# Kernel tuning notes

Measured on AMD Instinct MI355X. Metric: run time of the kernel, lower is better.

Reference implementation:

```python
import jax, jax.numpy as jnp
import numpy as np

V, T, E, H, L, R = 50257, 1024, 768, 12, 6, 4
B = 2
D = E // H
NEG = -1e9


def layer_norm(x, w, b, eps=1e-5):
    m = jnp.mean(x, axis=-1, keepdims=True)
    v = jnp.var(x, axis=-1, keepdims=True)
    return (x - m) * jax.lax.rsqrt(v + eps) * w + b


def setup_inputs() -> dict:
    key = jax.random.key(0)
    ks = jax.random.split(key, 8)
    s = 0.02
    inp = {
        "x": jax.random.randint(ks[0], (B, T), 0, V, dtype=jnp.int64),
        "tok_emb": s * jax.random.normal(ks[1], (V, E), jnp.float32),
        "pos_emb": s * jax.random.normal(ks[2], (T, E), jnp.float32),
        "ln1_w": jnp.ones((L, E), jnp.float32),
        "ln1_b": jnp.zeros((L, E), jnp.float32),
        "qkv_w": s * jax.random.normal(ks[3], (L, E, 3 * E), jnp.float32),
        "qkv_b": jnp.zeros((L, 3 * E), jnp.float32),
        "out_w": s * jax.random.normal(ks[4], (L, E, E), jnp.float32),
        "out_b": jnp.zeros((L, E), jnp.float32),
        "ln2_w": jnp.ones((L, E), jnp.float32),
        "ln2_b": jnp.zeros((L, E), jnp.float32),
        "mlp_w1": s * jax.random.normal(ks[5], (L, E, R * E), jnp.float32),
        "mlp_b1": jnp.zeros((L, R * E), jnp.float32),
        "mlp_w2": s * jax.random.normal(ks[6], (L, R * E, E), jnp.float32),
        "mlp_b2": jnp.zeros((L, E), jnp.float32),
        "lnf_w": jnp.ones((E,), jnp.float32),
        "lnf_b": jnp.zeros((E,), jnp.float32),
        "head_w": s * jax.random.normal(ks[7], (E, V), jnp.float32),
    }
    return inp


def _gpt2(x, tok_emb, pos_emb, ln1_w, ln1_b, qkv_w, qkv_b, out_w, out_b,
          ln2_w, ln2_b, mlp_w1, mlp_b1, mlp_w2, mlp_b2, lnf_w, lnf_b, head_w):
    b, t = x.shape
    h = tok_emb[x] + pos_emb[:t][None]  # [B,T,E]; dropout = identity (eval)
    mask = jnp.tril(jnp.ones((t, t), bool))
    scale = 1.0 / np.sqrt(D)

    def block(h, p):
        l1w, l1b, qw, qb, ow, ob, l2w, l2b, w1, b1, w2, b2 = p
        hn = layer_norm(h, l1w, l1b)
        qkv = hn @ qw + qb  # [B,T,3E]
        q, k, v = jnp.split(qkv, 3, axis=-1)
        q = q.reshape(b, t, H, D).transpose(0, 2, 1, 3)  # [B,H,T,D]
        k = k.reshape(b, t, H, D).transpose(0, 2, 1, 3)
        v = v.reshape(b, t, H, D).transpose(0, 2, 1, 3)
        att = jnp.einsum('bhqd,bhkd->bhqk', q, k) * scale
        att = jnp.where(mask, att, NEG)
        att = jax.nn.softmax(att, axis=-1)  # att dropout = identity (eval)
        o = jnp.einsum('bhqk,bhkd->bhqd', att, v)
        o = o.transpose(0, 2, 1, 3).reshape(b, t, E)
        h = h + (o @ ow + ob)  # res dropout = identity
        hn2 = layer_norm(h, l2w, l2b)
        m = jax.nn.gelu(hn2 @ w1 + b1, approximate=False) @ w2 + b2
        return h + m, None

    layer_params = (ln1_w, ln1_b, qkv_w, qkv_b, out_w, out_b,
                    ln2_w, ln2_b, mlp_w1, mlp_b1, mlp_w2, mlp_b2)
    h, _ = jax.lax.scan(block, h, layer_params)
    h = layer_norm(h, lnf_w, lnf_b)
    return h @ head_w  # [B,T,V]


def reference(x, tok_emb, pos_emb, ln1_w, ln1_b, qkv_w, qkv_b, out_w, out_b,
              ln2_w, ln2_b, mlp_w1, mlp_b1, mlp_w2, mlp_b2, lnf_w, lnf_b, head_w):
    return _gpt2(x, tok_emb, pos_emb, ln1_w, ln1_b, qkv_w, qkv_b, out_w, out_b,
                 ln2_w, ln2_b, mlp_w1, mlp_b1, mlp_w2, mlp_b2, lnf_w, lnf_b, head_w)
```

## Files before the change

kernel.cpp:

```cpp
#include <hip/hip_runtime.h>
#include <hip/hip_bf16.h>
#include <math.h>
#include <stdint.h>


#define T_SEQ 1024
#define E_DIM 768
#define NHEAD 12
#define HDIM 64
#define NLAYER 6
#define VOCAB 50257
#define VPAD 50304
#define BT 2048

typedef __attribute__((ext_vector_type(8))) short bf16x8;
typedef __attribute__((ext_vector_type(4))) float f32x4;

static __device__ __forceinline__ ushort f2bf(float x) {
    uint u = __float_as_uint(x);
    uint r = (u + 0x7fffu + ((u >> 16) & 1u)) >> 16;
    return (ushort)r;
}
static __device__ __forceinline__ float bf2f(ushort u) {
    return __uint_as_float(((uint)u) << 16);
}

static __device__ __forceinline__ void gld16(const ushort* g, ushort* l) {
    __builtin_amdgcn_global_load_lds(
        (const __attribute__((address_space(1))) void*)g,
        (__attribute__((address_space(3))) void*)l, 16, 0, 0);
}

__global__ __launch_bounds__(192) void embed_k(const int* __restrict__ x,
                                               const float* __restrict__ tok,
                                               const float* __restrict__ pos,
                                               float* __restrict__ h) {
    int bt = blockIdx.x;
    int t = bt & (T_SEQ - 1);
    int id = x[bt];
    float4 a = ((const float4*)(tok + (size_t)id * E_DIM))[threadIdx.x];
    float4 b = ((const float4*)(pos + (size_t)t * E_DIM))[threadIdx.x];
    float4 r; r.x = a.x + b.x; r.y = a.y + b.y; r.z = a.z + b.z; r.w = a.w + b.w;
    ((float4*)(h + (size_t)bt * E_DIM))[threadIdx.x] = r;
}

__global__ __launch_bounds__(256) void ln_k(const float* __restrict__ in,
                                            const float* __restrict__ w,
                                            const float* __restrict__ b,
                                            ushort* __restrict__ oh,
                                            ushort* __restrict__ ol) {
    int rid = blockIdx.x;
    int tid = threadIdx.x;
    const float* rp = in + (size_t)rid * E_DIM;
    float x0 = rp[tid], x1 = rp[tid + 256], x2 = rp[tid + 512];
    float s = x0 + x1 + x2;
    float q = x0 * x0 + x1 * x1 + x2 * x2;
    #pragma unroll
    for (int off = 32; off >= 1; off >>= 1) {
        s += __shfl_down(s, off);
        q += __shfl_down(q, off);
    }
    __shared__ float ss[4], qq[4];
    int lane = tid & 63, wid = tid >> 6;
    if (lane == 0) { ss[wid] = s; qq[wid] = q; }
    __syncthreads();
    float S = ss[0] + ss[1] + ss[2] + ss[3];
    float Q = qq[0] + qq[1] + qq[2] + qq[3];
    float mean = S * (1.0f / E_DIM);
    float var = Q * (1.0f / E_DIM) - mean * mean;
    float inv = rsqrtf(var + 1e-5f);
    size_t ob = (size_t)rid * E_DIM;
    #pragma unroll
    for (int j = 0; j < 3; j++) {
        int c = tid + j * 256;
        float xv = (j == 0) ? x0 : (j == 1) ? x1 : x2;
        float y = (xv - mean) * inv * w[c] + b[c];
        ushort hh = f2bf(y);
        oh[ob + c] = hh;
        ol[ob + c] = f2bf(y - bf2f(hh));
    }
}

__global__ __launch_bounds__(256) void tconv_k(const float* __restrict__ W,
                                               ushort* __restrict__ Thi,
                                               ushort* __restrict__ Tlo,
                                               int K, int N, int Npad) {
    int k0 = blockIdx.x * 32, n0 = blockIdx.y * 32;
    __shared__ float tile[32][33];
    int t = threadIdx.x;
    int kr = t >> 3, nc = (t & 7) << 2;
    const float* wp = W + (size_t)(k0 + kr) * N + n0 + nc;
    #pragma unroll
    for (int j = 0; j < 4; j++)
        tile[kr][nc + j] = (n0 + nc + j < N) ? wp[j] : 0.f;
    __syncthreads();
    int nr = t >> 3, kc = (t & 7) << 2;
    ushort hv[4], lv[4];
    #pragma unroll
    for (int j = 0; j < 4; j++) {
        float x = tile[kc + j][nr];
        hv[j] = f2bf(x);
        lv[j] = f2bf(x - bf2f(hv[j]));
    }
    size_t ob = (size_t)(n0 + nr) * K + k0 + kc;
    uint2 ph, pl;
    ph.x = (uint)hv[0] | ((uint)hv[1] << 16); ph.y = (uint)hv[2] | ((uint)hv[3] << 16);
    pl.x = (uint)lv[0] | ((uint)lv[1] << 16); pl.y = (uint)lv[2] | ((uint)lv[3] << 16);
    *(uint2*)(Thi + ob) = ph;
    *(uint2*)(Tlo + ob) = pl;
}

template <int EPI>
__global__ __launch_bounds__(256) void gemmf_k(const ushort* __restrict__ Ahi,
                                               const ushort* __restrict__ Alo,
                                               const ushort* __restrict__ Bhi,
                                               const ushort* __restrict__ Blo,
                                               const float* __restrict__ bias,
                                               const float* __restrict__ res,
                                               float* __restrict__ C,
                                               ushort* __restrict__ Chi,
                                               ushort* __restrict__ Clo,
                                               int M, int N, int K) {
    __shared__ __align__(16) ushort lds[4 * 128 * 32];
    ushort* Ash = lds;
    ushort* Asl = lds + 4096;
    ushort* Bsh = lds + 8192;
    ushort* Bsl = lds + 12288;
    const int tid = threadIdx.x;
    const int lane = tid & 63;
    const int wave = tid >> 6;
    const int wm64 = (wave >> 1) * 64;
    const int wn64 = (wave & 1) * 64;
    const int lrow = lane & 15;
    const int lkc = lane >> 4;
    const int n0 = blockIdx.x * 128;
    const int m0 = blockIdx.y * 128;

    f32x4 acc[4][4];
    #pragma unroll
    for (int i = 0; i < 4; i++)
        #pragma unroll
        for (int j = 0; j < 4; j++)
            acc[i][j] = (f32x4){0.f, 0.f, 0.f, 0.f};

    const int r0s = wave * 16 + (lane >> 2);
    const int r1s = r0s + 64;
    const int c0s = ((lane & 3) ^ ((r0s >> 1) & 3)) << 3;
    const int c1s = ((lane & 3) ^ ((r1s >> 1) & 3)) << 3;
    const ushort* pAh0 = Ahi + (size_t)(m0 + r0s) * K + c0s;
    const ushort* pAh1 = Ahi + (size_t)(m0 + r1s) * K + c1s;
    const ushort* pAl0 = Alo + (size_t)(m0 + r0s) * K + c0s;
    const ushort* pAl1 = Alo + (size_t)(m0 + r1s) * K + c1s;
    const ushort* pBh0 = Bhi + (size_t)(n0 + r0s) * K + c0s;
    const ushort* pBh1 = Bhi + (size_t)(n0 + r1s) * K + c1s;
    const ushort* pBl0 = Blo + (size_t)(n0 + r0s) * K + c0s;
    const ushort* pBl1 = Blo + (size_t)(n0 + r1s) * K + c1s;
    ushort* dst0 = lds + (size_t)wave * 512;
    ushort* dst1 = lds + (size_t)(wave + 4) * 512;

    for (int k0 = 0; k0 < K; k0 += 32) {
        __syncthreads();
        gld16(pAh0 + k0, dst0);
        gld16(pAh1 + k0, dst1);
        gld16(pAl0 + k0, dst0 + 4096);
        gld16(pAl1 + k0, dst1 + 4096);
        gld16(pBh0 + k0, dst0 + 8192);
        gld16(pBh1 + k0, dst1 + 8192);
        gld16(pBl0 + k0, dst0 + 12288);
        gld16(pBl1 + k0, dst1 + 12288);
        __syncthreads();

        bf16x8 ah[4], al[4], bh[4], bl[4];
        #pragma unroll
        for (int f = 0; f < 4; f++) {
            int arow = wm64 + (f << 4) + lrow;
            int aoff = (arow << 5) + ((lkc ^ ((arow >> 1) & 3)) << 3);
            ah[f] = *(const bf16x8*)&Ash[aoff];
            al[f] = *(const bf16x8*)&Asl[aoff];
            int brow = wn64 + (f << 4) + lrow;
            int boff = (brow << 5) + ((lkc ^ ((brow >> 1) & 3)) << 3);
            bh[f] = *(const bf16x8*)&Bsh[boff];
            bl[f] = *(const bf16x8*)&Bsl[boff];
        }
        #pragma unroll
        for (int mf = 0; mf < 4; mf++)
            #pragma unroll
            for (int nf = 0; nf < 4; nf++) {
                acc[mf][nf] = __builtin_amdgcn_mfma_f32_16x16x32_bf16(
                    ah[mf], bh[nf], acc[mf][nf], 0, 0, 0);
                acc[mf][nf] = __builtin_amdgcn_mfma_f32_16x16x32_bf16(
                    ah[mf], bl[nf], acc[mf][nf], 0, 0, 0);
                acc[mf][nf] = __builtin_amdgcn_mfma_f32_16x16x32_bf16(
                    al[mf], bh[nf], acc[mf][nf], 0, 0, 0);
            }
    }

    const int colb = n0 + wn64 + (lane & 15);
    const int rowb = m0 + wm64 + ((lane >> 4) << 2);
    #pragma unroll
    for (int nf = 0; nf < 4; nf++) {
        int col = colb + nf * 16;
        if (col >= N) continue;
        float bv = bias ? bias[col] : 0.f;
        #pragma unroll
        for (int mf = 0; mf < 4; mf++) {
            f32x4 v = acc[mf][nf];
            #pragma unroll
            for (int q = 0; q < 4; q++) {
                int row = rowb + mf * 16 + q;
                size_t idx = (size_t)row * N + col;
                float x = v[q] + bv;
                if (EPI == 1) {
                    x = 0.5f * x * (1.0f + erff(x * 0.70710678118654752f));
                    ushort hh = f2bf(x);
                    Chi[idx] = hh;
                    Clo[idx] = f2bf(x - bf2f(hh));
                } else if (EPI == 2) {
                    x += res[idx];
                    C[idx] = x;
                } else {
                    C[idx] = x;
                }
            }
        }
    }
}

__global__ __launch_bounds__(256) void attn_k(const float* __restrict__ qkv,
                                              ushort* __restrict__ oh,
                                              ushort* __restrict__ ol) {
    const int qt = blockIdx.x;
    const int hh = blockIdx.y;
    const int bb = blockIdx.z;
    const int tid = threadIdx.x;
    __shared__ __align__(16) float Qs[64][68];
    __shared__ __align__(16) float Ks[64][68];
    __shared__ __align__(16) float Vs[64][68];
    __shared__ __align__(16) float Ssm[64][68];
    __shared__ float m_s[64], l_s[64], f_s[64];

    const int q0 = qt * 64;
    const size_t base = (size_t)bb * T_SEQ * (3 * E_DIM);
    const int hoff = hh * HDIM;

    #pragma unroll
    for (int j = 0; j < 4; j++) {
        int s = tid + j * 256;
        int rr = s >> 4, c4 = (s & 15) << 2;
        *(float4*)&Qs[rr][c4] =
            *(const float4*)(qkv + base + (size_t)(q0 + rr) * (3 * E_DIM) + hoff + c4);
    }
    if (tid < 64) { m_s[tid] = -1e30f; l_s[tid] = 0.f; }

    float acc[4][4] = {};
    const int r0 = (tid >> 4) << 2, c0 = (tid & 15) << 2;
    const int rs = tid >> 2, cq = (tid & 3) << 4;

    for (int kt = 0; kt <= qt; ++kt) {
        int k0 = kt * 64;
        __syncthreads();
        #pragma unroll
        for (int j = 0; j < 4; j++) {
            int s = tid + j * 256;
            int rr = s >> 4, c4 = (s & 15) << 2;
            const float* kp = qkv + base + (size_t)(k0 + rr) * (3 * E_DIM) + hoff;
            *(float4*)&Ks[rr][c4] = *(const float4*)(kp + E_DIM + c4);
            *(float4*)&Vs[rr][c4] = *(const float4*)(kp + 2 * E_DIM + c4);
        }
        __syncthreads();

        float sacc[4][4] = {};
        #pragma unroll
        for (int d0 = 0; d0 < 64; d0 += 4) {
            float qf[4][4], kf[4][4];
            #pragma unroll
            for (int i = 0; i < 4; i++) {
                float4 v = *(const float4*)&Qs[r0 + i][d0];
                qf[i][0] = v.x; qf[i][1] = v.y; qf[i][2] = v.z; qf[i][3] = v.w;
            }
            #pragma unroll
            for (int j = 0; j < 4; j++) {
                float4 v = *(const float4*)&Ks[c0 + j][d0];
                kf[j][0] = v.x; kf[j][1] = v.y; kf[j][2] = v.z; kf[j][3] = v.w;
            }
            #pragma unroll
            for (int i = 0; i < 4; i++)
                #pragma unroll
                for (int j = 0; j < 4; j++)
                    #pragma unroll
                    for (int d = 0; d < 4; d++)
                        sacc[i][j] = fmaf(qf[i][d], kf[j][d], sacc[i][j]);
        }
        bool diag = (kt == qt);
        #pragma unroll
        for (int i = 0; i < 4; i++) {
            float4 w;
            float vv[4];
            #pragma unroll
            for (int j = 0; j < 4; j++) {
                float v = sacc[i][j] * 0.125f;
                if (diag && (c0 + j) > (r0 + i)) v = -1e9f;
                vv[j] = v;
            }
            w.x = vv[0]; w.y = vv[1]; w.z = vv[2]; w.w = vv[3];
            *(float4*)&Ssm[r0 + i][c0] = w;
        }
        __syncthreads();

        float mx = -1e30f;
        #pragma unroll
        for (int c = 0; c < 16; c++) mx = fmaxf(mx, Ssm[rs][cq + c]);
        mx = fmaxf(mx, __shfl_xor(mx, 1));
        mx = fmaxf(mx, __shfl_xor(mx, 2));
        float m_old = m_s[rs];
        float m_new = fmaxf(m_old, mx);
        float ps = 0.f;
        #pragma unroll
        for (int c = 0; c < 16; c++) {
            float p = expf(Ssm[rs][cq + c] - m_new);
            Ssm[rs][cq + c] = p;
            ps += p;
        }
        ps += __shfl_xor(ps, 1);
        ps += __shfl_xor(ps, 2);
        if ((tid & 3) == 0) {
            float f = expf(m_old - m_new);
            l_s[rs] = l_s[rs] * f + ps;
            m_s[rs] = m_new;
            f_s[rs] = f;
        }
        __syncthreads();

        #pragma unroll
        for (int i = 0; i < 4; i++) {
            float f = f_s[r0 + i];
            #pragma unroll
            for (int j = 0; j < 4; j++) acc[i][j] *= f;
        }
        #pragma unroll 8
        for (int k = 0; k < 64; k++) {
            float4 vv = *(const float4*)&Vs[k][c0];
            float vf[4] = {vv.x, vv.y, vv.z, vv.w};
            float pv[4];
            #pragma unroll
            for (int i = 0; i < 4; i++) pv[i] = Ssm[r0 + i][k];
            #pragma unroll
            for (int i = 0; i < 4; i++)
                #pragma unroll
                for (int j = 0; j < 4; j++)
                    acc[i][j] = fmaf(pv[i], vf[j], acc[i][j]);
        }
    }

    #pragma unroll
    for (int i = 0; i < 4; i++) {
        float inv = 1.0f / l_s[r0 + i];
        size_t idx = (size_t)(bb * T_SEQ + q0 + r0 + i) * E_DIM + hoff + c0;
        ushort hv[4], lv[4];
        #pragma unroll
        for (int j = 0; j < 4; j++) {
            float v = acc[i][j] * inv;
            hv[j] = f2bf(v);
            lv[j] = f2bf(v - bf2f(hv[j]));
        }
        uint2 ph, pl;
        ph.x = (uint)hv[0] | ((uint)hv[1] << 16); ph.y = (uint)hv[2] | ((uint)hv[3] << 16);
        pl.x = (uint)lv[0] | ((uint)lv[1] << 16); pl.y = (uint)lv[2] | ((uint)lv[3] << 16);
        *(uint2*)(oh + idx) = ph;
        *(uint2*)(ol + idx) = pl;
    }
}

static inline char* al256(char* p) {
    return (char*)(((uintptr_t)p + 255) & ~(uintptr_t)255);
}

extern "C" void kernel_launch(void* const* d_in, const int* in_sizes, int n_in,
                              void* d_out, int out_size, void* d_ws, size_t ws_size,
                              hipStream_t stream) {
    const int* x        = (const int*)d_in[0];
    const float* tok    = (const float*)d_in[1];
    const float* pos    = (const float*)d_in[2];
    const float* ln1_w  = (const float*)d_in[3];
    const float* ln1_b  = (const float*)d_in[4];
    const float* qkv_w  = (const float*)d_in[5];
    const float* qkv_b  = (const float*)d_in[6];
    const float* out_w  = (const float*)d_in[7];
    const float* out_b  = (const float*)d_in[8];
    const float* ln2_w  = (const float*)d_in[9];
    const float* ln2_b  = (const float*)d_in[10];
    const float* mlp_w1 = (const float*)d_in[11];
    const float* mlp_b1 = (const float*)d_in[12];
    const float* mlp_w2 = (const float*)d_in[13];
    const float* mlp_b2 = (const float*)d_in[14];
    const float* lnf_w  = (const float*)d_in[15];
    const float* lnf_b  = (const float*)d_in[16];
    const float* head_w = (const float*)d_in[17];
    float* out = (float*)d_out;

    char* p = (char*)d_ws;
    float* h    = (float*)p;  p = al256(p + (size_t)BT * E_DIM * 4);
    float* qkvb = (float*)p;  p = al256(p + (size_t)BT * 3 * E_DIM * 4);
    ushort* hnh = (ushort*)p; p = al256(p + (size_t)BT * E_DIM * 2);
    ushort* hnl = (ushort*)p; p = al256(p + (size_t)BT * E_DIM * 2);
    ushort* obh = (ushort*)p; p = al256(p + (size_t)BT * E_DIM * 2);
    ushort* obl = (ushort*)p; p = al256(p + (size_t)BT * E_DIM * 2);
    ushort* m1h = (ushort*)p; p = al256(p + (size_t)BT * 4 * E_DIM * 2);
    ushort* m1l = (ushort*)p; p = al256(p + (size_t)BT * 4 * E_DIM * 2);
    ushort* qTh = (ushort*)p; p = al256(p + (size_t)3 * E_DIM * E_DIM * 2);
    ushort* qTl = (ushort*)p; p = al256(p + (size_t)3 * E_DIM * E_DIM * 2);
    ushort* oTh = (ushort*)p; p = al256(p + (size_t)E_DIM * E_DIM * 2);
    ushort* oTl = (ushort*)p; p = al256(p + (size_t)E_DIM * E_DIM * 2);
    ushort* w1h = (ushort*)p; p = al256(p + (size_t)4 * E_DIM * E_DIM * 2);
    ushort* w1l = (ushort*)p; p = al256(p + (size_t)4 * E_DIM * E_DIM * 2);
    ushort* w2h = (ushort*)p; p = al256(p + (size_t)4 * E_DIM * E_DIM * 2);
    ushort* w2l = (ushort*)p; p = al256(p + (size_t)4 * E_DIM * E_DIM * 2);
    ushort* hTh = (ushort*)p; p = al256(p + (size_t)VPAD * E_DIM * 2);
    ushort* hTl = (ushort*)p; p = al256(p + (size_t)VPAD * E_DIM * 2);

    embed_k<<<BT, 192, 0, stream>>>(x, tok, pos, h);

    for (int l = 0; l < NLAYER; ++l) {
        tconv_k<<<dim3(E_DIM / 32, 3 * E_DIM / 32), 256, 0, stream>>>(
            qkv_w + (size_t)l * E_DIM * 3 * E_DIM, qTh, qTl,
            E_DIM, 3 * E_DIM, 3 * E_DIM);
        tconv_k<<<dim3(E_DIM / 32, E_DIM / 32), 256, 0, stream>>>(
            out_w + (size_t)l * E_DIM * E_DIM, oTh, oTl, E_DIM, E_DIM, E_DIM);
        tconv_k<<<dim3(E_DIM / 32, 4 * E_DIM / 32), 256, 0, stream>>>(
            mlp_w1 + (size_t)l * E_DIM * 4 * E_DIM, w1h, w1l,
            E_DIM, 4 * E_DIM, 4 * E_DIM);
        tconv_k<<<dim3(4 * E_DIM / 32, E_DIM / 32), 256, 0, stream>>>(
            mlp_w2 + (size_t)l * 4 * E_DIM * E_DIM, w2h, w2l,
            4 * E_DIM, E_DIM, E_DIM);

        ln_k<<<BT, 256, 0, stream>>>(h, ln1_w + l * E_DIM, ln1_b + l * E_DIM,
                                     hnh, hnl);
        gemmf_k<0><<<dim3(3 * E_DIM / 128, BT / 128), 256, 0, stream>>>(
            hnh, hnl, qTh, qTl, qkv_b + (size_t)l * 3 * E_DIM, nullptr,
            qkvb, nullptr, nullptr, BT, 3 * E_DIM, E_DIM);
        attn_k<<<dim3(T_SEQ / 64, NHEAD, 2), 256, 0, stream>>>(qkvb, obh, obl);
        gemmf_k<2><<<dim3(E_DIM / 128, BT / 128), 256, 0, stream>>>(
            obh, obl, oTh, oTl, out_b + (size_t)l * E_DIM, h,
            h, nullptr, nullptr, BT, E_DIM, E_DIM);
        ln_k<<<BT, 256, 0, stream>>>(h, ln2_w + l * E_DIM, ln2_b + l * E_DIM,
                                     hnh, hnl);
        gemmf_k<1><<<dim3(4 * E_DIM / 128, BT / 128), 256, 0, stream>>>(
            hnh, hnl, w1h, w1l, mlp_b1 + (size_t)l * 4 * E_DIM, nullptr,
            nullptr, m1h, m1l, BT, 4 * E_DIM, E_DIM);
        gemmf_k<2><<<dim3(E_DIM / 128, BT / 128), 256, 0, stream>>>(
            m1h, m1l, w2h, w2l, mlp_b2 + (size_t)l * E_DIM, h,
            h, nullptr, nullptr, BT, E_DIM, 4 * E_DIM);
    }

    tconv_k<<<dim3(E_DIM / 32, VPAD / 32), 256, 0, stream>>>(
        head_w, hTh, hTl, E_DIM, VOCAB, VPAD);
    ln_k<<<BT, 256, 0, stream>>>(h, lnf_w, lnf_b, hnh, hnl);
    gemmf_k<0><<<dim3(VPAD / 128, BT / 128), 256, 0, stream>>>(
        hnh, hnl, hTh, hTl, nullptr, nullptr,
        out, nullptr, nullptr, BT, VOCAB, E_DIM);
}
```

Baseline: 4.478 ms.

## Split-K small GEMMs, batch weight conversion, swizzle GEMM blocks, vectorize attention softmax

The output-projection and MLP-down GEMMs now use split-K (2 and 8 slices) writing partial sums, which a new reduction kernel adds to the residual together with the bias. These GEMMs previously launched only 96 workgroups. When the workspace is large enough, all layers' weight transposes and conversions run in batched launches up front instead of per layer. GEMM workgroups are remapped across groups of 8 for better cache locality, and the attention softmax and PV loops use float4 LDS accesses with __expf. The cost is extra partial-sum traffic, an added reduction kernel, and slightly less precise exponentials.

```diff
diff --git a/kernel.cpp b/kernel.cpp
--- a/kernel.cpp
+++ b/kernel.cpp
@@ -85,6 +85,10 @@
                                                ushort* __restrict__ Thi,
                                                ushort* __restrict__ Tlo,
                                                int K, int N, int Npad) {
+    int l = blockIdx.z;
+    W   += (size_t)l * K * N;
+    Thi += (size_t)l * Npad * K;
+    Tlo += (size_t)l * Npad * K;
     int k0 = blockIdx.x * 32, n0 = blockIdx.y * 32;
     __shared__ float tile[32][33];
     int t = threadIdx.x;
@@ -133,8 +137,19 @@
     const int wn64 = (wave & 1) * 64;
     const int lrow = lane & 15;
     const int lkc = lane >> 4;
-    const int n0 = blockIdx.x * 128;
-    const int m0 = blockIdx.y * 128;
+
+    int gx = gridDim.x, gy = gridDim.y;
+    int nwg = gx * gy;
+    int lin = blockIdx.y * gx + blockIdx.x;
+    int bx, by;
+    if ((nwg & 7) == 0) {
+        int chunk = nwg >> 3;
+        int logical = (lin & 7) * chunk + (lin >> 3);
+        bx = logical / gy;
+        by = logical % gy;
+    } else { bx = blockIdx.x; by = blockIdx.y; }
+    const int n0 = bx * 128;
+    const int m0 = by * 128;
 
     f32x4 acc[4][4];
     #pragma unroll
@@ -158,7 +173,15 @@
     ushort* dst0 = lds + (size_t)wave * 512;
     ushort* dst1 = lds + (size_t)(wave + 4) * 512;
 
-    for (int k0 = 0; k0 < K; k0 += 32) {
+    int kz = 0, kbeg = 0, kend = K;
+    if (EPI == 3) {
+        kz = blockIdx.z;
+        int Ks = K / gridDim.z;
+        kbeg = kz * Ks;
+        kend = kbeg + Ks;
+    }
+
+    for (int k0 = kbeg; k0 < kend; k0 += 32) {
         __syncthreads();
         gld16(pAh0 + k0, dst0);
         gld16(pAh1 + k0, dst1);
@@ -197,6 +220,7 @@
 
     const int colb = n0 + wn64 + (lane & 15);
     const int rowb = m0 + wm64 + ((lane >> 4) << 2);
+    const size_t pbase = (EPI == 3) ? (size_t)kz * M * N : 0;
     #pragma unroll
     for (int nf = 0; nf < 4; nf++) {
         int col = colb + nf * 16;
@@ -218,12 +242,30 @@
                 } else if (EPI == 2) {
                     x += res[idx];
                     C[idx] = x;
+                } else if (EPI == 3) {
+                    C[pbase + idx] = x;
                 } else {
                     C[idx] = x;
                 }
             }
         }
     }
+}
+
+__global__ __launch_bounds__(256) void redres_k(const float* __restrict__ P,
+                                                const float* __restrict__ bias,
+                                                float* __restrict__ h,
+                                                int MN, int N, int KZ) {
+    int i = (blockIdx.x * 256 + threadIdx.x) * 4;
+    if (i >= MN) return;
+    float4 s = *(const float4*)(h + i);
+    float4 b = *(const float4*)(bias + (i % N));
+    s.x += b.x; s.y += b.y; s.z += b.z; s.w += b.w;
+    for (int z = 0; z < KZ; z++) {
+        float4 pv = *(const float4*)(P + (size_t)z * MN + i);
+        s.x += pv.x; s.y += pv.y; s.z += pv.z; s.w += pv.w;
+    }
+    *(float4*)(h + i) = s;
 }
 
 __global__ __launch_bounds__(256) void attn_k(const float* __restrict__ qkv,
@@ -307,24 +349,33 @@
         }
         __syncthreads();
 
+        float4 sv[4];
+        #pragma unroll
+        for (int c4 = 0; c4 < 4; c4++)
+            sv[c4] = *(const float4*)&Ssm[rs][cq + c4 * 4];
         float mx = -1e30f;
         #pragma unroll
-        for (int c = 0; c < 16; c++) mx = fmaxf(mx, Ssm[rs][cq + c]);
+        for (int c4 = 0; c4 < 4; c4++)
+            mx = fmaxf(fmaxf(fmaxf(mx, sv[c4].x), fmaxf(sv[c4].y, sv[c4].z)),
+                       sv[c4].w);
         mx = fmaxf(mx, __shfl_xor(mx, 1));
         mx = fmaxf(mx, __shfl_xor(mx, 2));
         float m_old = m_s[rs];
         float m_new = fmaxf(m_old, mx);
         float ps = 0.f;
         #pragma unroll
-        for (int c = 0; c < 16; c++) {
-            float p = expf(Ssm[rs][cq + c] - m_new);
-            Ssm[rs][cq + c] = p;
-            ps += p;
+        for (int c4 = 0; c4 < 4; c4++) {
+            sv[c4].x = __expf(sv[c4].x - m_new);
+            sv[c4].y = __expf(sv[c4].y - m_new);
+            sv[c4].z = __expf(sv[c4].z - m_new);
+            sv[c4].w = __expf(sv[c4].w - m_new);
+            ps += sv[c4].x + sv[c4].y + sv[c4].z + sv[c4].w;
+            *(float4*)&Ssm[rs][cq + c4 * 4] = sv[c4];
         }
         ps += __shfl_xor(ps, 1);
         ps += __shfl_xor(ps, 2);
         if ((tid & 3) == 0) {
-            float f = expf(m_old - m_new);
+            float f = __expf(m_old - m_new);
             l_s[rs] = l_s[rs] * f + ps;
             m_s[rs] = m_new;
             f_s[rs] = f;
@@ -337,18 +388,24 @@
             #pragma unroll
             for (int j = 0; j < 4; j++) acc[i][j] *= f;
         }
-        #pragma unroll 8
-        for (int k = 0; k < 64; k++) {
-            float4 vv = *(const float4*)&Vs[k][c0];
-            float vf[4] = {vv.x, vv.y, vv.z, vv.w};
-            float pv[4];
-            #pragma unroll
-            for (int i = 0; i < 4; i++) pv[i] = Ssm[r0 + i][k];
-            #pragma unroll
-            for (int i = 0; i < 4; i++)
+        #pragma unroll 4
+        for (int k4 = 0; k4 < 64; k4 += 4) {
+            float4 pr[4], vr[4];
+            #pragma unroll
+            for (int i = 0; i < 4; i++) pr[i] = *(const float4*)&Ssm[r0 + i][k4];
+            #pragma unroll
+            for (int d = 0; d < 4; d++) vr[d] = *(const float4*)&Vs[k4 + d][c0];
+            #pragma unroll
+            for (int i = 0; i < 4; i++) {
+                float pf[4] = {pr[i].x, pr[i].y, pr[i].z, pr[i].w};
                 #pragma unroll
-                for (int j = 0; j < 4; j++)
-                    acc[i][j] = fmaf(pv[i], vf[j], acc[i][j]);
+                for (int d = 0; d < 4; d++) {
+                    acc[i][0] = fmaf(pf[d], vr[d].x, acc[i][0]);
+                    acc[i][1] = fmaf(pf[d], vr[d].y, acc[i][1]);
+                    acc[i][2] = fmaf(pf[d], vr[d].z, acc[i][2]);
+                    acc[i][3] = fmaf(pf[d], vr[d].w, acc[i][3]);
+                }
+            }
         }
     }
 
@@ -398,62 +455,145 @@
     const float* head_w = (const float*)d_in[17];
     float* out = (float*)d_out;
 
-    char* p = (char*)d_ws;
-    float* h    = (float*)p;  p = al256(p + (size_t)BT * E_DIM * 4);
-    float* qkvb = (float*)p;  p = al256(p + (size_t)BT * 3 * E_DIM * 4);
-    ushort* hnh = (ushort*)p; p = al256(p + (size_t)BT * E_DIM * 2);
-    ushort* hnl = (ushort*)p; p = al256(p + (size_t)BT * E_DIM * 2);
-    ushort* obh = (ushort*)p; p = al256(p + (size_t)BT * E_DIM * 2);
-    ushort* obl = (ushort*)p; p = al256(p + (size_t)BT * E_DIM * 2);
-    ushort* m1h = (ushort*)p; p = al256(p + (size_t)BT * 4 * E_DIM * 2);
-    ushort* m1l = (ushort*)p; p = al256(p + (size_t)BT * 4 * E_DIM * 2);
-    ushort* qTh = (ushort*)p; p = al256(p + (size_t)3 * E_DIM * E_DIM * 2);
-    ushort* qTl = (ushort*)p; p = al256(p + (size_t)3 * E_DIM * E_DIM * 2);
-    ushort* oTh = (ushort*)p; p = al256(p + (size_t)E_DIM * E_DIM * 2);
-    ushort* oTl = (ushort*)p; p = al256(p + (size_t)E_DIM * E_DIM * 2);
-    ushort* w1h = (ushort*)p; p = al256(p + (size_t)4 * E_DIM * E_DIM * 2);
-    ushort* w1l = (ushort*)p; p = al256(p + (size_t)4 * E_DIM * E_DIM * 2);
-    ushort* w2h = (ushort*)p; p = al256(p + (size_t)4 * E_DIM * E_DIM * 2);
-    ushort* w2l = (ushort*)p; p = al256(p + (size_t)4 * E_DIM * E_DIM * 2);
-    ushort* hTh = (ushort*)p; p = al256(p + (size_t)VPAD * E_DIM * 2);
-    ushort* hTl = (ushort*)p; p = al256(p + (size_t)VPAD * E_DIM * 2);
+    const size_t Zh   = (size_t)BT * E_DIM * 4;
+    const size_t Zqkv = (size_t)BT * 3 * E_DIM * 4;
+    const size_t Zbf  = (size_t)BT * E_DIM * 2;
+    const size_t Zm1  = (size_t)BT * 4 * E_DIM * 2;
+    const size_t ZP   = (size_t)8 * BT * E_DIM * 4;
+    const size_t ZqT  = (size_t)3 * E_DIM * E_DIM * 2;
+    const size_t ZoT  = (size_t)E_DIM * E_DIM * 2;
+    const size_t Zw1T = (size_t)4 * E_DIM * E_DIM * 2;
+    const size_t Zw2T = (size_t)4 * E_DIM * E_DIM * 2;
+    const size_t ZhT  = (size_t)VPAD * E_DIM * 2;
+
+    char* base = (char*)d_ws;
+    char* p = base;
+    auto take = [&](size_t bytes) { char* r = p; p = al256(p + bytes); return r; };
+
+    float*  h    = (float*)take(Zh);
+    float*  qkvb = (float*)take(Zqkv);
+    ushort* hnh  = (ushort*)take(Zbf);
+    ushort* hnl  = (ushort*)take(Zbf);
+    ushort* obh  = (ushort*)take(Zbf);
+    ushort* obl  = (ushort*)take(Zbf);
+    ushort* m1h  = (ushort*)take(Zm1);
+    ushort* m1l  = (ushort*)take(Zm1);
+    float*  Pbuf = (float*)take(ZP);
+    ushort* qTh  = (ushort*)take(ZqT * NLAYER);
+    ushort* qTl  = (ushort*)take(ZqT * NLAYER);
+    ushort* oTh  = (ushort*)take(ZoT * NLAYER);
+    ushort* oTl  = (ushort*)take(ZoT * NLAYER);
+    ushort* w1h  = (ushort*)take(Zw1T * NLAYER);
+    ushort* w1l  = (ushort*)take(Zw1T * NLAYER);
+    ushort* w2h  = (ushort*)take(Zw2T * NLAYER);
+    ushort* w2l  = (ushort*)take(Zw2T * NLAYER);
+    ushort* hTh  = (ushort*)take(ZhT);
+    ushort* hTl  = (ushort*)take(ZhT);
+    bool big = (size_t)(p - base) <= ws_size;
+
+    if (!big) {
+        p = base;
+        h    = (float*)take(Zh);
+        qkvb = (float*)take(Zqkv);
+        hnh  = (ushort*)take(Zbf);
+        hnl  = (ushort*)take(Zbf);
+        obh  = (ushort*)take(Zbf);
+        obl  = (ushort*)take(Zbf);
+        m1h  = (ushort*)take(Zm1);
+        m1l  = (ushort*)take(Zm1);
+        qTh  = (ushort*)take(ZqT);
+        qTl  = (ushort*)take(ZqT);
+        oTh  = (ushort*)take(ZoT);
+        oTl  = (ushort*)take(ZoT);
+        w1h  = (ushort*)take(Zw1T);
+        w1l  = (ushort*)take(Zw1T);
+        w2h  = (ushort*)take(Zw2T);
+        w2l  = (ushort*)take(Zw2T);
+        hTh  = (ushort*)take(ZhT);
+        hTl  = (ushort*)take(ZhT);
+        Pbuf = nullptr;
+    }
+
+    if (big) {
+        tconv_k<<<dim3(E_DIM / 32, 3 * E_DIM / 32, NLAYER), 256, 0, stream>>>(
+            qkv_w, qTh, qTl, E_DIM, 3 * E_DIM, 3 * E_DIM);
+        tconv_k<<<dim3(E_DIM / 32, E_DIM / 32, NLAYER), 256, 0, stream>>>(
+            out_w, oTh, oTl, E_DIM, E_DIM, E_DIM);
+        tconv_k<<<dim3(E_DIM / 32, 4 * E_DIM / 32, NLAYER), 256, 0, stream>>>(
+            mlp_w1, w1h, w1l, E_DIM, 4 * E_DIM, 4 * E_DIM);
+        tconv_k<<<dim3(4 * E_DIM / 32, E_DIM / 32, NLAYER), 256, 0, stream>>>(
+            mlp_w2, w2h, w2l, 4 * E_DIM, E_DIM, E_DIM);
+        tconv_k<<<dim3(E_DIM / 32, VPAD / 32, 1), 256, 0, stream>>>(
+            head_w, hTh, hTl, E_DIM, VOCAB, VPAD);
+    }
 
     embed_k<<<BT, 192, 0, stream>>>(x, tok, pos, h);
 
     for (int l = 0; l < NLAYER; ++l) {
-        tconv_k<<<dim3(E_DIM / 32, 3 * E_DIM / 32), 256, 0, stream>>>(
-            qkv_w + (size_t)l * E_DIM * 3 * E_DIM, qTh, qTl,
-            E_DIM, 3 * E_DIM, 3 * E_DIM);
-        tconv_k<<<dim3(E_DIM / 32, E_DIM / 32), 256, 0, stream>>>(
-            out_w + (size_t)l * E_DIM * E_DIM, oTh, oTl, E_DIM, E_DIM, E_DIM);
-        tconv_k<<<dim3(E_DIM / 32, 4 * E_DIM / 32), 256, 0, stream>>>(
-            mlp_w1 + (size_t)l * E_DIM * 4 * E_DIM, w1h, w1l,
-            E_DIM, 4 * E_DIM, 4 * E_DIM);
-        tconv_k<<<dim3(4 * E_DIM / 32, E_DIM / 32), 256, 0, stream>>>(
-            mlp_w2 + (size_t)l * 4 * E_DIM * E_DIM, w2h, w2l,
-            4 * E_DIM, E_DIM, E_DIM);
+        const ushort *qThl, *qTll, *oThl, *oTll, *w1hl, *w1ll, *w2hl, *w2ll;
+        if (big) {
+            qThl = qTh + (size_t)l * (ZqT / 2);  qTll = qTl + (size_t)l * (ZqT / 2);
+            oThl = oTh + (size_t)l * (ZoT / 2);  oTll = oTl + (size_t)l * (ZoT / 2);
+            w1hl = w1h + (size_t)l * (Zw1T / 2); w1ll = w1l + (size_t)l * (Zw1T / 2);
+            w2hl = w2h + (size_t)l * (Zw2T / 2); w2ll = w2l + (size_t)l * (Zw2T / 2);
+        } else {
+            tconv_k<<<dim3(E_DIM / 32, 3 * E_DIM / 32, 1), 256, 0, stream>>>(
+                qkv_w + (size_t)l * E_DIM * 3 * E_DIM, qTh, qTl,
+                E_DIM, 3 * E_DIM, 3 * E_DIM);
+            tconv_k<<<dim3(E_DIM / 32, E_DIM / 32, 1), 256, 0, stream>>>(
+                out_w + (size_t)l * E_DIM * E_DIM, oTh, oTl, E_DIM, E_DIM, E_DIM);
+            tconv_k<<<dim3(E_DIM / 32, 4 * E_DIM / 32, 1), 256, 0, stream>>>(
+                mlp_w1 + (size_t)l * E_DIM * 4 * E_DIM, w1h, w1l,
+                E_DIM, 4 * E_DIM, 4 * E_DIM);
+            tconv_k<<<dim3(4 * E_DIM / 32, E_DIM / 32, 1), 256, 0, stream>>>(
+                mlp_w2 + (size_t)l * 4 * E_DIM * E_DIM, w2h, w2l,
+                4 * E_DIM, E_DIM, E_DIM);
+            qThl = qTh; qTll = qTl; oThl = oTh; oTll = oTl;
+            w1hl = w1h; w1ll = w1l; w2hl = w2h; w2ll = w2l;
+        }
 
         ln_k<<<BT, 256, 0, stream>>>(h, ln1_w + l * E_DIM, ln1_b + l * E_DIM,
                                      hnh, hnl);
         gemmf_k<0><<<dim3(3 * E_DIM / 128, BT / 128), 256, 0, stream>>>(
-            hnh, hnl, qTh, qTl, qkv_b + (size_t)l * 3 * E_DIM, nullptr,
+            hnh, hnl, qThl, qTll, qkv_b + (size_t)l * 3 * E_DIM, nullptr,
             qkvb, nullptr, nullptr, BT, 3 * E_DIM, E_DIM);
         attn_k<<<dim3(T_SEQ / 64, NHEAD, 2), 256, 0, stream>>>(qkvb, obh, obl);
-        gemmf_k<2><<<dim3(E_DIM / 128, BT / 128), 256, 0, stream>>>(
-            obh, obl, oTh, oTl, out_b + (size_t)l * E_DIM, h,
-            h, nullptr, nullptr, BT, E_DIM, E_DIM);
+
+        if (big) {
+            gemmf_k<3><<<dim3(E_DIM / 128, BT / 128, 2), 256, 0, stream>>>(
+                obh, obl, oThl, oTll, nullptr, nullptr,
+                Pbuf, nullptr, nullptr, BT, E_DIM, E_DIM);
+            redres_k<<<(BT * E_DIM / 4 + 255) / 256, 256, 0, stream>>>(
+                Pbuf, out_b + (size_t)l * E_DIM, h, BT * E_DIM, E_DIM, 2);
+        } else {
+            gemmf_k<2><<<dim3(E_DIM / 128, BT / 128), 256, 0, stream>>>(
+                obh, obl, oThl, oTll, out_b + (size_t)l * E_DIM, h,
+                h, nullptr, nullptr, BT, E_DIM, E_DIM);
+        }
+
         ln_k<<<BT, 256, 0, stream>>>(h, ln2_w + l * E_DIM, ln2_b + l * E_DIM,
                                      hnh, hnl);
         gemmf_k<1><<<dim3(4 * E_DIM / 128, BT / 128), 256, 0, stream>>>(
-            hnh, hnl, w1h, w1l, mlp_b1 + (size_t)l * 4 * E_DIM, nullptr,
+            hnh, hnl, w1hl, w1ll, mlp_b1 + (size_t)l * 4 * E_DIM, nullptr,
             nullptr, m1h, m1l, BT, 4 * E_DIM, E_DIM);
-        gemmf_k<2><<<dim3(E_DIM / 128, BT / 128), 256, 0, stream>>>(
-            m1h, m1l, w2h, w2l, mlp_b2 + (size_t)l * E_DIM, h,
-            h, nullptr, nullptr, BT, E_DIM, 4 * E_DIM);
-    }
-
-    tconv_k<<<dim3(E_DIM / 32, VPAD / 32), 256, 0, stream>>>(
-        head_w, hTh, hTl, E_DIM, VOCAB, VPAD);
+
+        if (big) {
+            gemmf_k<3><<<dim3(E_DIM / 128, BT / 128, 8), 256, 0, stream>>>(
+                m1h, m1l, w2hl, w2ll, nullptr, nullptr,
+                Pbuf, nullptr, nullptr, BT, E_DIM, 4 * E_DIM);
+            redres_k<<<(BT * E_DIM / 4 + 255) / 256, 256, 0, stream>>>(
+                Pbuf, mlp_b2 + (size_t)l * E_DIM, h, BT * E_DIM, E_DIM, 8);
+        } else {
+            gemmf_k<2><<<dim3(E_DIM / 128, BT / 128), 256, 0, stream>>>(
+                m1h, m1l, w2hl, w2ll, mlp_b2 + (size_t)l * E_DIM, h,
+                h, nullptr, nullptr, BT, E_DIM, 4 * E_DIM);
+        }
+    }
+
+    if (!big) {
+        tconv_k<<<dim3(E_DIM / 32, VPAD / 32, 1), 256, 0, stream>>>(
+            head_w, hTh, hTl, E_DIM, VOCAB, VPAD);
+    }
     ln_k<<<BT, 256, 0, stream>>>(h, lnf_w, lnf_b, hnh, hnl);
     gemmf_k<0><<<dim3(VPAD / 128, BT / 128), 256, 0, stream>>>(
         hnh, hnl, hTh, hTl, nullptr, nullptr,
```

New measurement: 3.997 ms. 1.12x faster.
